# Kernel tuning notes

Hardware: AMD Instinct MI355X
Metric: run time of the kernel (lower is better)

## Reference

```python
import jax, jax.numpy as jnp
import numpy as np

NH = 16   # n_heads
HD = 64   # head_size
EMB = 1024  # n_embd = NH * HD
B, T = 4, 2048


def setup_inputs() -> dict:
    key = jax.random.key(0)
    k1, k2, k3 = jax.random.split(key, 3)
    x = jax.random.normal(k1, (B, T, EMB), dtype=jnp.float32)
    # torch Linear(in, out, bias=False): weight [out,in]; we store transposed [in,out]
    W_attn = jax.random.normal(k2, (EMB, 3 * NH * HD), dtype=jnp.float32) * (EMB ** -0.5)
    W_proj = jax.random.normal(k3, (NH * HD, EMB), dtype=jnp.float32) * ((NH * HD) ** -0.5)
    b_proj = jnp.zeros((EMB,), dtype=jnp.float32)
    return {"x": x, "W_attn": W_attn, "W_proj": W_proj, "b_proj": b_proj}


def reference(x, W_attn, W_proj, b_proj):
    Bq, Tq, C = x.shape
    qkv = x @ W_attn                      # [B,T,3*Nh*H]
    qs, ks, vs = jnp.split(qkv, 3, axis=2)
    def to_heads(t):                      # [B,T,Nh*H] -> [B,Nh,T,H]
        return t.reshape(Bq, Tq, NH, HD).transpose(0, 2, 1, 3)
    q, k, v = to_heads(qs), to_heads(ks), to_heads(vs)
    scores = jnp.einsum('bnth,bnsh->bnts', q, k) * (HD ** -0.5)  # [B,Nh,T,T]
    causal = jnp.tril(jnp.ones((Tq, Tq), dtype=bool))
    scores = jnp.where(causal, scores, -jnp.inf)
    attn = jax.nn.softmax(scores, axis=-1)
    # dropout is identity in eval mode
    y = jnp.einsum('bnts,bnsh->bnth', attn, v)                   # [B,Nh,T,H]
    y = y.transpose(0, 2, 1, 3).reshape(Bq, Tq, NH * HD)
    return y @ W_proj + b_proj
```

## Files before the change

kernel.cpp:

```cpp
#include <hip/hip_runtime.h>
#include <hip/hip_bf16.h>

#define NH 16
#define HD 64
#define EMB 1024
#define BB 4
#define TT 2048
#define MTOT (BB*TT)
#define N1 (3*NH*HD)
#define KD EMB

#define QSCALE 0.18033688011112042f
#define FMAX 14.0f

typedef __bf16 bf16x8 __attribute__((ext_vector_type(8)));
typedef __bf16 bf16x4 __attribute__((ext_vector_type(4)));
typedef float  f32x4  __attribute__((ext_vector_type(4)));
typedef __hip_bfloat16 hbf;

__device__ __forceinline__ void async_copy16(const hbf* g, hbf* l) {
    __builtin_amdgcn_global_load_lds(
        (const __attribute__((address_space(1))) void*)g,
        (__attribute__((address_space(3))) void*)l, 16, 0, 0);
}

__device__ __forceinline__ bf16x4 pack4(float x0, float x1, float x2, float x3) {
    union { bf16x4 v; hbf a[4]; } u;
    u.a[0] = __float2bfloat16(x0);
    u.a[1] = __float2bfloat16(x1);
    u.a[2] = __float2bfloat16(x2);
    u.a[3] = __float2bfloat16(x3);
    return u.v;
}


__global__ __launch_bounds__(256) void f32_to_bf16_v4(const float* __restrict__ in,
                                                      hbf* __restrict__ out, int n4) {
    int i = blockIdx.x * blockDim.x + threadIdx.x;
    if (i < n4) {
        float4 v = ((const float4*)in)[i];
        *(bf16x4*)(out + 4 * (size_t)i) = pack4(v.x, v.y, v.z, v.w);
    }
}

__global__ __launch_bounds__(256) void f32_to_bf16_T(const float* __restrict__ in,
                                                     hbf* __restrict__ out, int R, int C) {
    __shared__ float T[64][65];
    int bc = blockIdx.x % (C / 64), br = blockIdx.x / (C / 64);
    int r0 = br * 64, c0 = bc * 64;
    int tr = threadIdx.x >> 6, tc = threadIdx.x & 63;
    #pragma unroll
    for (int i = 0; i < 16; ++i)
        T[4 * i + tr][tc] = in[(size_t)(r0 + 4 * i + tr) * C + c0 + tc];
    __syncthreads();
    #pragma unroll
    for (int i = 0; i < 16; ++i)
        out[(size_t)(c0 + 4 * i + tr) * R + r0 + tc] = __float2bfloat16(T[tc][4 * i + tr]);
}


template<int NBN, int MODE>
__global__ __launch_bounds__(256, 4) void gemm_v2(
    const hbf* __restrict__ A, const hbf* __restrict__ Bt,
    hbf* __restrict__ qh, hbf* __restrict__ kh, hbf* __restrict__ vt,
    const float* __restrict__ bias, float* __restrict__ out)
{
    constexpr int NKT = KD / 32;
    __shared__ __align__(16) hbf As[2 * 128 * 32];
    __shared__ __align__(16) hbf Bs[2 * 128 * 32];

    int tid = threadIdx.x;
    int wv = tid >> 6, lane = tid & 63;
    int g = lane >> 4, c = lane & 15;
    int wm = wv >> 1, wn = wv & 1;
    int wg = (blockIdx.x & 7) * (8 * NBN) + (blockIdx.x >> 3);
    int bn = wg % NBN, bm = wg / NBN;
    int m0 = bm * 128, n0 = bn * 128;

    int sr = tid >> 2;
    int sgc = (tid & 3) ^ (sr & 3);
    const hbf* Asrc0 = A  + (size_t)(m0 + sr) * KD + sgc * 8;
    const hbf* Asrc1 = A  + (size_t)(m0 + 64 + sr) * KD + sgc * 8;
    const hbf* Bsrc0 = Bt + (size_t)(n0 + sr) * KD + sgc * 8;
    const hbf* Bsrc1 = Bt + (size_t)(n0 + 64 + sr) * KD + sgc * 8;
    int ld0 = (tid & ~63) * 8, ld1 = 2048 + (tid & ~63) * 8;

#define STG(tt, buf) { \
    async_copy16(Asrc0 + (tt) * 32, As + (buf) * 4096 + ld0); \
    async_copy16(Asrc1 + (tt) * 32, As + (buf) * 4096 + ld1); \
    async_copy16(Bsrc0 + (tt) * 32, Bs + (buf) * 4096 + ld0); \
    async_copy16(Bsrc1 + (tt) * 32, Bs + (buf) * 4096 + ld1); }

    int x3 = c & 3;
    int ao = (wm * 64 + c) * 32 + ((g ^ x3) << 3);
    int bo = (wn * 64 + c) * 32 + ((g ^ x3) << 3);

    f32x4 acc[4][4];
    #pragma unroll
    for (int i = 0; i < 4; ++i)
        #pragma unroll
        for (int j = 0; j < 4; ++j) acc[i][j] = (f32x4){0.f, 0.f, 0.f, 0.f};

    STG(0, 0);
    STG(1, 1);
    asm volatile("s_waitcnt vmcnt(4)" ::: "memory");
    asm volatile("s_barrier" ::: "memory");
    __builtin_amdgcn_sched_barrier(0);

    for (int t = 0; t < NKT; ++t) {
        int cur = t & 1;
        const hbf* Ab = As + cur * 4096;
        const hbf* Bb = Bs + cur * 4096;
        bf16x8 af[4], bfr[4];
        #pragma unroll
        for (int i = 0; i < 4; ++i) af[i] = *(const bf16x8*)(Ab + ao + i * 512);
        #pragma unroll
        for (int j = 0; j < 4; ++j) bfr[j] = *(const bf16x8*)(Bb + bo + j * 512);
        asm volatile("s_waitcnt lgkmcnt(0)" ::: "memory");
        __builtin_amdgcn_sched_barrier(0);
        asm volatile("s_barrier" ::: "memory");
        __builtin_amdgcn_sched_barrier(0);
        if (t + 2 < NKT) STG(t + 2, cur);
        __builtin_amdgcn_s_setprio(1);
        #pragma unroll
        for (int i = 0; i < 4; ++i)
            #pragma unroll
            for (int j = 0; j < 4; ++j)
                acc[i][j] = __builtin_amdgcn_mfma_f32_16x16x32_bf16(af[i], bfr[j], acc[i][j], 0, 0, 0);
        __builtin_amdgcn_s_setprio(0);
        if (t + 2 < NKT) { asm volatile("s_waitcnt vmcnt(4)" ::: "memory"); }
        else             { asm volatile("s_waitcnt vmcnt(0)" ::: "memory"); }
        asm volatile("s_barrier" ::: "memory");
        __builtin_amdgcn_sched_barrier(0);
    }
#undef STG

    if constexpr (MODE == 0) {
        int colbase = n0 + wn * 64;
        int which = colbase >> 10;
        int h = (colbase & 1023) >> 6;
        int b = m0 / TT;
        int trow = (m0 % TT) + wm * 64;
        if (which < 2) {
            float scale = (which == 0) ? QSCALE : 1.0f;
            hbf* dst = ((which == 0) ? qh : kh) + ((size_t)b * NH + h) * TT * HD;
            #pragma unroll
            for (int i = 0; i < 4; ++i)
                #pragma unroll
                for (int j = 0; j < 4; ++j) {
                    int d = j * 16 + c;
                    #pragma unroll
                    for (int r = 0; r < 4; ++r) {
                        int trw = trow + i * 16 + g * 4 + r;
                        dst[(size_t)trw * HD + d] = __float2bfloat16(acc[i][j][r] * scale);
                    }
                }
        } else {
            hbf* dst = vt + ((size_t)b * NH + h) * TT * HD;
            #pragma unroll
            for (int i = 0; i < 4; ++i)
                #pragma unroll
                for (int j = 0; j < 4; ++j) {
                    int d = j * 16 + c;
                    #pragma unroll
                    for (int r = 0; r < 4; ++r) {
                        int trw = trow + i * 16 + g * 4 + r;
                        dst[(size_t)d * TT + trw] = __float2bfloat16(acc[i][j][r]);
                    }
                }
        }
    } else {
        #pragma unroll
        for (int i = 0; i < 4; ++i)
            #pragma unroll
            for (int j = 0; j < 4; ++j) {
                int col = n0 + wn * 64 + j * 16 + c;
                float bv = bias[col];
                #pragma unroll
                for (int r = 0; r < 4; ++r) {
                    int row = m0 + wm * 64 + i * 16 + g * 4 + r;
                    out[(size_t)row * EMB + col] = acc[i][j][r] + bv;
                }
            }
    }
}


__global__ __launch_bounds__(512, 6) void attn(
    const hbf* __restrict__ qh, const hbf* __restrict__ kh, const hbf* __restrict__ vt,
    hbf* __restrict__ y)
{
    __shared__ __align__(16) hbf Ks[2 * 64 * 64];
    __shared__ __align__(16) hbf Vs[2 * 64 * 64];
    __shared__ __align__(16) hbf Ps[8][16 * 64];

    int tid = threadIdx.x;
    int wv = tid >> 6, lane = tid & 63;
    int g = lane >> 4, c = lane & 15;
    int c7 = c & 7;

    int bidx = blockIdx.x;
    int bh = (bidx & 7) | (((bidx >> 7) & 7) << 3);
    int sst = 15 - ((bidx >> 3) & 15);
    int b = bh >> 4, h = bh & 15;
    int qb = sst * 128;
    int q0 = qb + wv * 16;
    int kend = q0 + 16;
    int nt = 2 * sst + 2;

    const hbf* Q = qh + (size_t)bh * TT * HD;
    const hbf* K = kh + (size_t)bh * TT * HD;
    const hbf* V = vt + (size_t)bh * TT * HD;
    hbf* Pq = &Ps[wv][0];

    int skey = tid >> 3, schunk = tid & 7;
    int sswz = (schunk ^ (skey & 7)) * 8;
    const hbf* Ksrc = K + (size_t)skey * HD + sswz;
    const hbf* Vsrc = V + (size_t)skey * TT + sswz;
    int sdst = (tid & ~63) * 8;

#define ASTG(tt, buf) { \
    async_copy16(Ksrc + (size_t)(tt) * 64 * HD, Ks + (buf) * 4096 + sdst); \
    async_copy16(Vsrc + (tt) * 64, Vs + (buf) * 4096 + sdst); }

    bf16x8 aq0 = *(const bf16x8*)(Q + (size_t)(q0 + c) * HD + g * 8);
    bf16x8 aq1 = *(const bf16x8*)(Q + (size_t)(q0 + c) * HD + 32 + g * 8);

    union { bf16x8 v; hbf a[8]; } uo;
    #pragma unroll
    for (int i = 0; i < 8; ++i) uo.a[i] = __float2bfloat16(1.0f);
    const bf16x8 ones8 = uo.v;

    f32x4 lacc = (f32x4){0.f, 0.f, 0.f, 0.f};
    f32x4 o[4];
    #pragma unroll
    for (int d = 0; d < 4; ++d) o[d] = (f32x4){0.f, 0.f, 0.f, 0.f};

    ASTG(0, 0);
    ASTG(1, 1);
    asm volatile("s_waitcnt vmcnt(2)" ::: "memory");
    asm volatile("s_barrier" ::: "memory");
    __builtin_amdgcn_sched_barrier(0);

    for (int tt = 0; tt < nt; ++tt) {
        int cur = tt & 1;
        int k0 = tt * 64;
        const hbf* Kb = Ks + cur * 4096;
        const hbf* Vb = Vs + cur * 4096;
        if (k0 < kend) {
            f32x4 s[4];
            #pragma unroll
            for (int t4 = 0; t4 < 4; ++t4) {
                int kt = k0 + 16 * t4;
                if (kt < kend) {
                    int rb = (16 * t4 + c) * 64;
                    bf16x8 kf0 = *(const bf16x8*)(Kb + rb + ((g ^ c7) << 3));
                    bf16x8 kf1 = *(const bf16x8*)(Kb + rb + (((4 + g) ^ c7) << 3));
                    f32x4 a = (f32x4){-FMAX, -FMAX, -FMAX, -FMAX};
                    a = __builtin_amdgcn_mfma_f32_16x16x32_bf16(kf0, aq0, a, 0, 0, 0);
                    a = __builtin_amdgcn_mfma_f32_16x16x32_bf16(kf1, aq1, a, 0, 0, 0);
                    if (kt == q0) {
                        #pragma unroll
                        for (int r = 0; r < 4; ++r)
                            a[r] = (g * 4 + r <= c) ? a[r] : -1e30f;
                    }
                    s[t4] = a;
                } else
                    s[t4] = (f32x4){-1e30f, -1e30f, -1e30f, -1e30f};
            }
            #pragma unroll
            for (int t4 = 0; t4 < 4; ++t4) {
                f32x4 e;
                #pragma unroll
                for (int r = 0; r < 4; ++r) e[r] = __builtin_amdgcn_exp2f(s[t4][r]);
                *(bf16x4*)(Pq + c * 64 + (((2 * t4 + (g >> 1)) ^ c7) << 3) + ((g & 1) << 2)) =
                    pack4(e[0], e[1], e[2], e[3]);
            }
            #pragma unroll
            for (int sc = 0; sc < 2; ++sc) {
                if (k0 + 32 * sc < kend) {
                    bf16x8 pf = *(const bf16x8*)(Pq + c * 64 + (((4 * sc + g) ^ c7) << 3));
                    lacc = __builtin_amdgcn_mfma_f32_16x16x32_bf16(ones8, pf, lacc, 0, 0, 0);
                    #pragma unroll
                    for (int d = 0; d < 4; ++d) {
                        bf16x8 vf = *(const bf16x8*)(Vb + (d * 16 + c) * 64 +
                                      (((4 * sc + g) ^ c7) << 3));
                        o[d] = __builtin_amdgcn_mfma_f32_16x16x32_bf16(vf, pf, o[d], 0, 0, 0);
                    }
                }
            }
        }
        asm volatile("s_barrier" ::: "memory");
        __builtin_amdgcn_sched_barrier(0);
        if (tt + 2 < nt) ASTG(tt + 2, cur);
        if (tt + 2 < nt) { asm volatile("s_waitcnt vmcnt(2)" ::: "memory"); }
        else             { asm volatile("s_waitcnt vmcnt(0)" ::: "memory"); }
        asm volatile("s_barrier" ::: "memory");
        __builtin_amdgcn_sched_barrier(0);
    }
#undef ASTG

    float inv = 1.0f / lacc[0];
    #pragma unroll
    for (int d = 0; d < 4; ++d) {
        *(bf16x4*)(y + (size_t)(b * TT + q0 + c) * EMB + h * HD + d * 16 + g * 4) =
            pack4(o[d][0] * inv, o[d][1] * inv, o[d][2] * inv, o[d][3] * inv);
    }
}


extern "C" void kernel_launch(void* const* d_in, const int* in_sizes, int n_in,
                              void* d_out, int out_size, void* d_ws, size_t ws_size,
                              hipStream_t stream)
{
    const float* x      = (const float*)d_in[0];
    const float* W_attn = (const float*)d_in[1];
    const float* W_proj = (const float*)d_in[2];
    const float* b_proj = (const float*)d_in[3];
    float* out = (float*)d_out;

    char* ws = (char*)d_ws;
    hbf* xb    = (hbf*)ws; ws += (size_t)MTOT * KD * 2;
    hbf* wab_t = (hbf*)ws; ws += (size_t)N1 * KD * 2;
    hbf* wpb_t = (hbf*)ws; ws += (size_t)EMB * EMB * 2;
    hbf* qh    = (hbf*)ws; ws += (size_t)MTOT * EMB * 2;
    hbf* kh    = (hbf*)ws; ws += (size_t)MTOT * EMB * 2;
    hbf* vt    = (hbf*)ws; ws += (size_t)MTOT * EMB * 2;
    hbf* yb    = (hbf*)ws; ws += (size_t)MTOT * EMB * 2;

    f32_to_bf16_v4<<<(MTOT * KD / 4 + 255) / 256, 256, 0, stream>>>(x, xb, MTOT * KD / 4);
    f32_to_bf16_T<<<(KD / 64) * (N1 / 64), 256, 0, stream>>>(W_attn, wab_t, KD, N1);
    f32_to_bf16_T<<<(KD / 64) * (EMB / 64), 256, 0, stream>>>(W_proj, wpb_t, KD, EMB);

    gemm_v2<N1 / 128, 0><<<(MTOT / 128) * (N1 / 128), 256, 0, stream>>>(
        xb, wab_t, qh, kh, vt, nullptr, nullptr);
    attn<<<BB * NH * 16, 512, 0, stream>>>(qh, kh, vt, yb);
    gemm_v2<EMB / 128, 1><<<(MTOT / 128) * (EMB / 128), 256, 0, stream>>>(
        yb, wpb_t, nullptr, nullptr, nullptr, b_proj, out);
}
```

Measured before the change: 266.8 us.

## Pair causal query blocks per workgroup and stage 128-key K/V tiles

```diff
diff --git a/kernel.cpp b/kernel.cpp
--- a/kernel.cpp
+++ b/kernel.cpp
@@ -186,12 +186,12 @@
 }
 
 
-__global__ __launch_bounds__(512, 6) void attn(
+__global__ __launch_bounds__(512, 4) void attn(
     const hbf* __restrict__ qh, const hbf* __restrict__ kh, const hbf* __restrict__ vt,
     hbf* __restrict__ y)
 {
-    __shared__ __align__(16) hbf Ks[2 * 64 * 64];
-    __shared__ __align__(16) hbf Vs[2 * 64 * 64];
+    __shared__ __align__(16) hbf Ks[2 * 128 * 64];
+    __shared__ __align__(16) hbf Vs[2 * 64 * 128];
     __shared__ __align__(16) hbf Ps[8][16 * 64];
 
     int tid = threadIdx.x;
@@ -200,112 +200,135 @@
     int c7 = c & 7;
 
     int bidx = blockIdx.x;
-    int bh = (bidx & 7) | (((bidx >> 7) & 7) << 3);
-    int sst = 15 - ((bidx >> 3) & 15);
+    int bh = (bidx & 7) | (((bidx >> 6) & 7) << 3);
+    int pi = (bidx >> 3) & 7;
     int b = bh >> 4, h = bh & 15;
-    int qb = sst * 128;
-    int q0 = qb + wv * 16;
-    int kend = q0 + 16;
-    int nt = 2 * sst + 2;
 
     const hbf* Q = qh + (size_t)bh * TT * HD;
     const hbf* K = kh + (size_t)bh * TT * HD;
     const hbf* V = vt + (size_t)bh * TT * HD;
     hbf* Pq = &Ps[wv][0];
 
-    int skey = tid >> 3, schunk = tid & 7;
-    int sswz = (schunk ^ (skey & 7)) * 8;
-    const hbf* Ksrc = K + (size_t)skey * HD + sswz;
-    const hbf* Vsrc = V + (size_t)skey * TT + sswz;
-    int sdst = (tid & ~63) * 8;
-
-#define ASTG(tt, buf) { \
-    async_copy16(Ksrc + (size_t)(tt) * 64 * HD, Ks + (buf) * 4096 + sdst); \
-    async_copy16(Vsrc + (tt) * 64, Vs + (buf) * 4096 + sdst); }
-
-    bf16x8 aq0 = *(const bf16x8*)(Q + (size_t)(q0 + c) * HD + g * 8);
-    bf16x8 aq1 = *(const bf16x8*)(Q + (size_t)(q0 + c) * HD + 32 + g * 8);
+#define ASTG(ss, buf) { \
+    int k0s = (ss) * 128; \
+    _Pragma("unroll") for (int it = 0; it < 2; ++it) { \
+        int e = it * 4096 + tid * 8; \
+        int key = e >> 6, sblk = (e >> 3) & 7; \
+        int dblk = sblk ^ (key & 7); \
+        async_copy16(K + (size_t)(k0s + key) * HD + dblk * 8, \
+                     Ks + (buf) * 8192 + it * 4096 + (tid & ~63) * 8); } \
+    _Pragma("unroll") for (int it = 0; it < 2; ++it) { \
+        int e = it * 4096 + tid * 8; \
+        int dim = e >> 7, kb = (e >> 3) & 15; \
+        int skb = kb ^ (dim & 7); \
+        async_copy16(V + (size_t)dim * TT + k0s + skb * 8, \
+                     Vs + (buf) * 8192 + it * 4096 + (tid & ~63) * 8); } }
 
     union { bf16x8 v; hbf a[8]; } uo;
     #pragma unroll
     for (int i = 0; i < 8; ++i) uo.a[i] = __float2bfloat16(1.0f);
     const bf16x8 ones8 = uo.v;
 
-    f32x4 lacc = (f32x4){0.f, 0.f, 0.f, 0.f};
-    f32x4 o[4];
-    #pragma unroll
-    for (int d = 0; d < 4; ++d) o[d] = (f32x4){0.f, 0.f, 0.f, 0.f};
-
-    ASTG(0, 0);
-    ASTG(1, 1);
-    asm volatile("s_waitcnt vmcnt(2)" ::: "memory");
-    asm volatile("s_barrier" ::: "memory");
-    __builtin_amdgcn_sched_barrier(0);
-
-    for (int tt = 0; tt < nt; ++tt) {
-        int cur = tt & 1;
-        int k0 = tt * 64;
-        const hbf* Kb = Ks + cur * 4096;
-        const hbf* Vb = Vs + cur * 4096;
-        if (k0 < kend) {
-            f32x4 s[4];
-            #pragma unroll
-            for (int t4 = 0; t4 < 4; ++t4) {
-                int kt = k0 + 16 * t4;
-                if (kt < kend) {
-                    int rb = (16 * t4 + c) * 64;
-                    bf16x8 kf0 = *(const bf16x8*)(Kb + rb + ((g ^ c7) << 3));
-                    bf16x8 kf1 = *(const bf16x8*)(Kb + rb + (((4 + g) ^ c7) << 3));
-                    f32x4 a = (f32x4){-FMAX, -FMAX, -FMAX, -FMAX};
-                    a = __builtin_amdgcn_mfma_f32_16x16x32_bf16(kf0, aq0, a, 0, 0, 0);
-                    a = __builtin_amdgcn_mfma_f32_16x16x32_bf16(kf1, aq1, a, 0, 0, 0);
-                    if (kt == q0) {
-                        #pragma unroll
-                        for (int r = 0; r < 4; ++r)
-                            a[r] = (g * 4 + r <= c) ? a[r] : -1e30f;
-                    }
-                    s[t4] = a;
-                } else
-                    s[t4] = (f32x4){-1e30f, -1e30f, -1e30f, -1e30f};
-            }
-            #pragma unroll
-            for (int t4 = 0; t4 < 4; ++t4) {
-                f32x4 e;
-                #pragma unroll
-                for (int r = 0; r < 4; ++r) e[r] = __builtin_amdgcn_exp2f(s[t4][r]);
-                *(bf16x4*)(Pq + c * 64 + (((2 * t4 + (g >> 1)) ^ c7) << 3) + ((g & 1) << 2)) =
-                    pack4(e[0], e[1], e[2], e[3]);
-            }
-            #pragma unroll
-            for (int sc = 0; sc < 2; ++sc) {
-                if (k0 + 32 * sc < kend) {
-                    bf16x8 pf = *(const bf16x8*)(Pq + c * 64 + (((4 * sc + g) ^ c7) << 3));
-                    lacc = __builtin_amdgcn_mfma_f32_16x16x32_bf16(ones8, pf, lacc, 0, 0, 0);
-                    #pragma unroll
-                    for (int d = 0; d < 4; ++d) {
-                        bf16x8 vf = *(const bf16x8*)(Vb + (d * 16 + c) * 64 +
-                                      (((4 * sc + g) ^ c7) << 3));
-                        o[d] = __builtin_amdgcn_mfma_f32_16x16x32_bf16(vf, pf, o[d], 0, 0, 0);
-                    }
-                }
-            }
+    #pragma unroll
+    for (int pass = 0; pass < 2; ++pass) {
+        int sst = pass ? (15 - pi) : pi;
+        int qb = sst * 128;
+        int q0 = qb + wv * 16;
+        int kend = q0 + 16;
+        int S = sst + 1;
+
+        bf16x8 aq0 = *(const bf16x8*)(Q + (size_t)(q0 + c) * HD + g * 8);
+        bf16x8 aq1 = *(const bf16x8*)(Q + (size_t)(q0 + c) * HD + 32 + g * 8);
+
+        f32x4 lacc = (f32x4){0.f, 0.f, 0.f, 0.f};
+        f32x4 o[4];
+        #pragma unroll
+        for (int d = 0; d < 4; ++d) o[d] = (f32x4){0.f, 0.f, 0.f, 0.f};
+
+        ASTG(0, 0);
+        if (S > 1) {
+            ASTG(1, 1);
+            asm volatile("s_waitcnt vmcnt(4)" ::: "memory");
+        } else {
+            asm volatile("s_waitcnt vmcnt(0)" ::: "memory");
         }
         asm volatile("s_barrier" ::: "memory");
         __builtin_amdgcn_sched_barrier(0);
-        if (tt + 2 < nt) ASTG(tt + 2, cur);
-        if (tt + 2 < nt) { asm volatile("s_waitcnt vmcnt(2)" ::: "memory"); }
-        else             { asm volatile("s_waitcnt vmcnt(0)" ::: "memory"); }
-        asm volatile("s_barrier" ::: "memory");
-        __builtin_amdgcn_sched_barrier(0);
+
+        for (int s = 0; s < S; ++s) {
+            int k0 = s * 128;
+            const hbf* Kb = Ks + (s & 1) * 8192;
+            const hbf* Vb = Vs + (s & 1) * 8192;
+
+            #pragma unroll
+            for (int ch = 0; ch < 2; ++ch) {
+                int c64 = k0 + ch * 64;
+                if (c64 < kend) {
+                    f32x4 sv[4];
+                    #pragma unroll
+                    for (int t = 0; t < 4; ++t) {
+                        int kt = c64 + 16 * t;
+                        if (kt < kend) {
+                            int rb = (ch * 64 + 16 * t + c) * 64;
+                            bf16x8 kf0 = *(const bf16x8*)(Kb + rb + ((g ^ c7) << 3));
+                            bf16x8 kf1 = *(const bf16x8*)(Kb + rb + (((4 + g) ^ c7) << 3));
+                            f32x4 a = (f32x4){-FMAX, -FMAX, -FMAX, -FMAX};
+                            a = __builtin_amdgcn_mfma_f32_16x16x32_bf16(kf0, aq0, a, 0, 0, 0);
+                            a = __builtin_amdgcn_mfma_f32_16x16x32_bf16(kf1, aq1, a, 0, 0, 0);
+                            if (kt == q0) {
+                                #pragma unroll
+                                for (int r = 0; r < 4; ++r)
+                                    a[r] = (g * 4 + r <= c) ? a[r] : -1e30f;
+                            }
+                            sv[t] = a;
+                        } else
+                            sv[t] = (f32x4){-1e30f, -1e30f, -1e30f, -1e30f};
+                    }
+                    #pragma unroll
+                    for (int t = 0; t < 4; ++t) {
+                        f32x4 e;
+                        #pragma unroll
+                        for (int r = 0; r < 4; ++r) e[r] = __builtin_amdgcn_exp2f(sv[t][r]);
+                        *(bf16x4*)(Pq + c * 64 + (((2 * t + (g >> 1)) ^ c7) << 3) + ((g & 1) << 2)) =
+                            pack4(e[0], e[1], e[2], e[3]);
+                    }
+                    #pragma unroll
+                    for (int sc = 0; sc < 2; ++sc) {
+                        if (c64 + 32 * sc < kend) {
+                            bf16x8 pf = *(const bf16x8*)(Pq + c * 64 + (((4 * sc + g) ^ c7) << 3));
+                            lacc = __builtin_amdgcn_mfma_f32_16x16x32_bf16(ones8, pf, lacc, 0, 0, 0);
+                            #pragma unroll
+                            for (int d = 0; d < 4; ++d) {
+                                int dim = d * 16 + c;
+                                bf16x8 vf = *(const bf16x8*)(Vb + dim * 128 +
+                                              (((ch * 8 + 4 * sc + g) ^ c7) << 3));
+                                o[d] = __builtin_amdgcn_mfma_f32_16x16x32_bf16(vf, pf, o[d], 0, 0, 0);
+                            }
+                        }
+                    }
+                }
+            }
+
+            asm volatile("s_barrier" ::: "memory");
+            __builtin_amdgcn_sched_barrier(0);
+            if (s + 2 < S) {
+                ASTG(s + 2, s & 1);
+                asm volatile("s_waitcnt vmcnt(4)" ::: "memory");
+            } else if (s + 1 < S) {
+                asm volatile("s_waitcnt vmcnt(0)" ::: "memory");
+            }
+            asm volatile("s_barrier" ::: "memory");
+            __builtin_amdgcn_sched_barrier(0);
+        }
+
+        float inv = 1.0f / lacc[0];
+        #pragma unroll
+        for (int d = 0; d < 4; ++d) {
+            *(bf16x4*)(y + (size_t)(b * TT + q0 + c) * EMB + h * HD + d * 16 + g * 4) =
+                pack4(o[d][0] * inv, o[d][1] * inv, o[d][2] * inv, o[d][3] * inv);
+        }
     }
 #undef ASTG
-
-    float inv = 1.0f / lacc[0];
-    #pragma unroll
-    for (int d = 0; d < 4; ++d) {
-        *(bf16x4*)(y + (size_t)(b * TT + q0 + c) * EMB + h * HD + d * 16 + g * 4) =
-            pack4(o[d][0] * inv, o[d][1] * inv, o[d][2] * inv, o[d][3] * inv);
-    }
 }
 
 
@@ -334,7 +357,7 @@
 
     gemm_v2<N1 / 128, 0><<<(MTOT / 128) * (N1 / 128), 256, 0, stream>>>(
         xb, wab_t, qh, kh, vt, nullptr, nullptr);
-    attn<<<BB * NH * 16, 512, 0, stream>>>(qh, kh, vt, yb);
+    attn<<<BB * NH * 8, 512, 0, stream>>>(qh, kh, vt, yb);
     gemm_v2<EMB / 128, 1><<<(MTOT / 128) * (EMB / 128), 256, 0, stream>>>(
         yb, wpb_t, nullptr, nullptr, nullptr, b_proj, out);
 }
```

Measured after the change: 250.9 us. 6.0% less time.
